# Kernel tuning notes

Hardware: AMD Instinct MI355X
Metric: run time of the kernel (lower is better)

The kernel has to match this reference:

```python
import jax, jax.numpy as jnp
import numpy as np

COSINE_SIM_SCALE = 8.0  # default scale in flash-cosine-sim-attention
LN_EPS = 1e-5
HEADS = 8

def _l2norm(t, eps=1e-12):
    return t * jax.lax.rsqrt(jnp.sum(t * t, axis=-1, keepdims=True) + eps)

def setup_inputs() -> dict:
    key = jax.random.key(0)
    k1, k2, k3 = jax.random.split(key, 3)
    b, n, dim = 2, 2048, 1024
    inner = 512  # heads * dim_head
    return {
        "x": jax.random.normal(k1, (b, n, dim), dtype=jnp.float32),
        "ln_w": jnp.ones((dim,), dtype=jnp.float32),
        "ln_b": jnp.zeros((dim,), dtype=jnp.float32),
        "w_qkv": jax.random.normal(k2, (dim, 3 * inner), dtype=jnp.float32) * 0.02,
        "w_out": jax.random.normal(k3, (inner, dim), dtype=jnp.float32) * 0.02,
    }

def reference(x, ln_w, ln_b, w_qkv, w_out):
    b, n, dim = x.shape
    h = HEADS
    # LayerNorm
    mu = jnp.mean(x, axis=-1, keepdims=True)
    var = jnp.mean(jnp.square(x - mu), axis=-1, keepdims=True)
    xn = (x - mu) * jax.lax.rsqrt(var + LN_EPS) * ln_w + ln_b
    # QKV projection, split into heads: b n (h d) -> b h n d
    qkv = xn @ w_qkv
    q, k, v = jnp.split(qkv, 3, axis=-1)
    def to_heads(t):
        return t.reshape(b, n, h, -1).transpose(0, 2, 1, 3)
    q, k, v = map(to_heads, (q, k, v))
    # cosine-sim attention: l2-normalize q, k then scaled dot product
    q = _l2norm(q)
    k = _l2norm(k)
    sim = jnp.einsum('bhid,bhjd->bhij', q, k) * COSINE_SIM_SCALE
    causal_mask = jnp.tril(jnp.ones((n, n), dtype=bool))
    sim = jnp.where(causal_mask, sim, jnp.finfo(sim.dtype).min)
    attn = jax.nn.softmax(sim, axis=-1)
    o = jnp.einsum('bhij,bhjd->bhid', attn, v)
    # b h n d -> b n (h d)
    o = o.transpose(0, 2, 1, 3).reshape(b, n, -1)
    return o @ w_out
```

## Files before the change

kernel.cpp:

```cpp
#include <hip/hip_runtime.h>
#include <hip/hip_bf16.h>

typedef __attribute__((ext_vector_type(8))) __bf16 bf16x8;
typedef __attribute__((ext_vector_type(4))) __bf16 bf16x4;
typedef __attribute__((ext_vector_type(4))) float f32x4;

#define B_     2
#define N_     2048
#define DIM_   1024
#define INNER_ 512
#define H_     8
#define DH_    64
#define ROWS_  (B_ * N_)
#define QKVN_  (3 * INNER_)
#define SEGROWS_ 5120
#define QSCALE_ 11.5415603f
#define MAXL2_  11.5415603f

static __device__ __forceinline__ f32x4 mfma16(bf16x8 a, bf16x8 b, f32x4 c) {
    return __builtin_amdgcn_mfma_f32_16x16x32_bf16(a, b, c, 0, 0, 0);
}

static __device__ __forceinline__ void gld_lds16(const void* g, void* l) {
    __builtin_amdgcn_global_load_lds((const __attribute__((address_space(1))) void*)g,
                                     (__attribute__((address_space(3))) void*)l, 16, 0, 0);
}

__global__ __launch_bounds__(256) void ln_kernel(const float* __restrict__ x,
                                                 const float* __restrict__ w,
                                                 const float* __restrict__ bb,
                                                 __bf16* __restrict__ xn) {
    int row = blockIdx.x;
    int tid = threadIdx.x;
    const float* xr = x + (size_t)row * DIM_;
    f32x4 xv = *reinterpret_cast<const f32x4*>(xr + tid * 4);
    float s  = xv.x + xv.y + xv.z + xv.w;
    float sq = xv.x * xv.x + xv.y * xv.y + xv.z * xv.z + xv.w * xv.w;
#pragma unroll
    for (int m = 1; m < 64; m <<= 1) {
        s  += __shfl_xor(s, m);
        sq += __shfl_xor(sq, m);
    }
    __shared__ float red[2][4];
    int wid = tid >> 6, lane = tid & 63;
    if (lane == 0) { red[0][wid] = s; red[1][wid] = sq; }
    __syncthreads();
    s  = red[0][0] + red[0][1] + red[0][2] + red[0][3];
    sq = red[1][0] + red[1][1] + red[1][2] + red[1][3];
    float mu   = s * (1.0f / DIM_);
    float var  = sq * (1.0f / DIM_) - mu * mu;
    float rstd = rsqrtf(var + 1e-5f);
    f32x4 wv = *reinterpret_cast<const f32x4*>(w  + tid * 4);
    f32x4 bv = *reinterpret_cast<const f32x4*>(bb + tid * 4);
    bf16x4 o;
#pragma unroll
    for (int j = 0; j < 4; ++j) o[j] = (__bf16)((xv[j] - mu) * rstd * wv[j] + bv[j]);
    *reinterpret_cast<bf16x4*>(xn + (size_t)row * DIM_ + tid * 4) = o;
}

__global__ __launch_bounds__(256) void transpose_both(const float* __restrict__ wqkv,
                                                      const float* __restrict__ wout,
                                                      __bf16* __restrict__ wqkvT,
                                                      __bf16* __restrict__ woutT) {
    __shared__ float t[64][65];
    int bid = blockIdx.x;
    const float* in; __bf16* out; int K, N, bx, by;
    if (bid < 384) { in = wqkv; out = wqkvT; K = DIM_;   N = QKVN_; bx = bid % 24; by = bid / 24; }
    else { bid -= 384; in = wout; out = woutT; K = INNER_; N = DIM_;  bx = bid % 16; by = bid / 16; }
    int n0 = bx * 64, k0 = by * 64;
    int w = threadIdx.x >> 6, lane = threadIdx.x & 63;
#pragma unroll
    for (int i = 0; i < 16; ++i) {
        int k = 16 * w + i;
        t[k][lane] = in[(size_t)(k0 + k) * N + n0 + lane];
    }
    __syncthreads();
#pragma unroll
    for (int i = 0; i < 16; ++i) {
        int n = 16 * w + i;
        out[(size_t)(n0 + n) * K + k0 + lane] = (__bf16)t[lane][n];
    }
}

__global__ __launch_bounds__(256) void gemm_qkv(const __bf16* __restrict__ A,
                                                const __bf16* __restrict__ Bt,
                                                __bf16* __restrict__ Qh,
                                                __bf16* __restrict__ Kh,
                                                __bf16* __restrict__ Vrow) {
    const int K = DIM_;
    __shared__ __bf16 As[2][128 * 32];
    __shared__ __bf16 Bs[2][128 * 32];
    int tid = threadIdx.x;
    int w = tid >> 6, lane = tid & 63;
    int lr = lane & 15, lg = lane >> 4;
    int m0 = blockIdx.y * 128, n0 = blockIdx.x * 128;
    int wm = (w >> 1) * 64, wn = (w & 1) * 64;
    int srow = tid >> 2, sc = tid & 3;
    const __bf16* Ab = A  + (size_t)m0 * K;
    const __bf16* Bb = Bt + (size_t)n0 * K;
    f32x4 acc[4][4];
#pragma unroll
    for (int mi = 0; mi < 4; ++mi)
#pragma unroll
        for (int ci = 0; ci < 4; ++ci) acc[mi][ci] = f32x4{0.f, 0.f, 0.f, 0.f};

    auto stage = [&](int buf, int k0) {
#pragma unroll
        for (int q = 0; q < 2; ++q) {
            int row = q * 64 + srow;
            int cs = sc ^ (row & 3);
            gld_lds16(Ab + (size_t)row * K + k0 + 8 * cs, &As[buf][(size_t)row * 32 + sc * 8]);
            gld_lds16(Bb + (size_t)row * K + k0 + 8 * cs, &Bs[buf][(size_t)row * 32 + sc * 8]);
        }
    };

    stage(0, 0);
    __syncthreads();
    int cur = 0;
    for (int k0 = 0; k0 < K; k0 += 32) {
        if (k0 + 32 < K) stage(cur ^ 1, k0 + 32);
        bf16x8 af[4], bfr[4];
#pragma unroll
        for (int mi = 0; mi < 4; ++mi) {
            int r = wm + 16 * mi + lr;
            af[mi] = *reinterpret_cast<const bf16x8*>(&As[cur][r * 32 + 8 * (lg ^ (r & 3))]);
        }
#pragma unroll
        for (int ci = 0; ci < 4; ++ci) {
            int r = wn + 16 * ci + lr;
            bfr[ci] = *reinterpret_cast<const bf16x8*>(&Bs[cur][r * 32 + 8 * (lg ^ (r & 3))]);
        }
#pragma unroll
        for (int mi = 0; mi < 4; ++mi)
#pragma unroll
            for (int ci = 0; ci < 4; ++ci)
                acc[mi][ci] = mfma16(af[mi], bfr[ci], acc[mi][ci]);
        __syncthreads();
        cur ^= 1;
    }
    int u = (n0 + wn) >> 6;
    bool isV = (u >= 16);
    float smul = (u < 8) ? QSCALE_ : 1.0f;
    __bf16* base;
    if (u < 8)       base = Qh   + (size_t)u * N_ * DH_;
    else if (u < 16) base = Kh   + (size_t)(u - 8) * N_ * DH_;
    else             base = Vrow + (size_t)(u - 16) * N_ * DH_;
#pragma unroll
    for (int mi = 0; mi < 4; ++mi)
#pragma unroll
        for (int r = 0; r < 4; ++r) {
            int grow = m0 + wm + 16 * mi + 4 * lg + r;
            int b = grow >> 11, n = grow & 2047;
            float sc2 = 1.0f;
            if (!isV) {
                float t = 0.f;
#pragma unroll
                for (int ci = 0; ci < 4; ++ci) t += acc[mi][ci][r] * acc[mi][ci][r];
#pragma unroll
                for (int m = 1; m < 16; m <<= 1) t += __shfl_xor(t, m);
                sc2 = rsqrtf(t + 1e-12f) * smul;
            }
            __bf16* dst = base + ((size_t)b * H_ * N_ + n) * DH_;
#pragma unroll
            for (int ci = 0; ci < 4; ++ci)
                dst[16 * ci + lr] = (__bf16)(acc[mi][ci][r] * sc2);
        }
}

__global__ __launch_bounds__(256) void gemm_out(const __bf16* __restrict__ A,
                                                const __bf16* __restrict__ Bt,
                                                float* __restrict__ C) {
    const int K = INNER_, N = DIM_;
    __shared__ __bf16 As[2][128 * 32];
    __shared__ __bf16 Bs[2][64 * 32];
    int tid = threadIdx.x;
    int w = tid >> 6, lane = tid & 63;
    int lr = lane & 15, lg = lane >> 4;
    int m0 = blockIdx.y * 128, n0 = blockIdx.x * 64;
    int wm = w * 32;
    int srow = tid >> 2, sc = tid & 3;
    const __bf16* Ab = A  + (size_t)m0 * K;
    const __bf16* Bb = Bt + (size_t)n0 * K;
    f32x4 acc[2][4];
#pragma unroll
    for (int mi = 0; mi < 2; ++mi)
#pragma unroll
        for (int ci = 0; ci < 4; ++ci) acc[mi][ci] = f32x4{0.f, 0.f, 0.f, 0.f};

    auto stage = [&](int buf, int k0) {
#pragma unroll
        for (int q = 0; q < 2; ++q) {
            int row = q * 64 + srow;
            int cs = sc ^ (row & 3);
            gld_lds16(Ab + (size_t)row * K + k0 + 8 * cs, &As[buf][(size_t)row * 32 + sc * 8]);
        }
        {
            int row = srow;
            int cs = sc ^ (row & 3);
            gld_lds16(Bb + (size_t)row * K + k0 + 8 * cs, &Bs[buf][(size_t)row * 32 + sc * 8]);
        }
    };

    stage(0, 0);
    __syncthreads();
    int cur = 0;
    for (int k0 = 0; k0 < K; k0 += 32) {
        if (k0 + 32 < K) stage(cur ^ 1, k0 + 32);
        bf16x8 af[2], bfr[4];
#pragma unroll
        for (int mi = 0; mi < 2; ++mi) {
            int r = wm + 16 * mi + lr;
            af[mi] = *reinterpret_cast<const bf16x8*>(&As[cur][r * 32 + 8 * (lg ^ (r & 3))]);
        }
#pragma unroll
        for (int ci = 0; ci < 4; ++ci) {
            int r = 16 * ci + lr;
            bfr[ci] = *reinterpret_cast<const bf16x8*>(&Bs[cur][r * 32 + 8 * (lg ^ (r & 3))]);
        }
#pragma unroll
        for (int mi = 0; mi < 2; ++mi)
#pragma unroll
            for (int ci = 0; ci < 4; ++ci)
                acc[mi][ci] = mfma16(af[mi], bfr[ci], acc[mi][ci]);
        __syncthreads();
        cur ^= 1;
    }
#pragma unroll
    for (int mi = 0; mi < 2; ++mi)
#pragma unroll
        for (int ci = 0; ci < 4; ++ci)
#pragma unroll
            for (int r = 0; r < 4; ++r)
                C[(size_t)(m0 + wm + 16 * mi + 4 * lg + r) * N + n0 + 16 * ci + lr] =
                    acc[mi][ci][r];
}

__global__ __launch_bounds__(256) void vtrans(const __bf16* __restrict__ Vrow,
                                              __bf16* __restrict__ Vt) {
    __shared__ __bf16 t[64][66];
    int bh = blockIdx.y, n0 = blockIdx.x * 64;
    int w = threadIdx.x >> 6, lane = threadIdx.x & 63;
#pragma unroll
    for (int i = 0; i < 16; ++i) {
        int nl = 16 * w + i;
        t[nl][lane] = Vrow[((size_t)bh * N_ + n0 + nl) * DH_ + lane];
    }
    __syncthreads();
#pragma unroll
    for (int i = 0; i < 16; ++i) {
        int d = 16 * w + i;
        Vt[(size_t)bh * DH_ * N_ + (size_t)d * N_ + n0 + lane] = t[lane][d];
    }
}

__global__ __launch_bounds__(256) void attn_kernel(const __bf16* __restrict__ Qh,
                                                   const __bf16* __restrict__ Kh,
                                                   const __bf16* __restrict__ Vt,
                                                   float* __restrict__ Opart,
                                                   float* __restrict__ lpart) {
    __shared__ __bf16 Ks[2][64 * 64];
    __shared__ __bf16 Vs[2][64 * 64];
    __shared__ __bf16 pl[4][16 * 64];
    int bh  = blockIdx.x & 15;
    int sid = blockIdx.x >> 4;
    int s, qt;
    if (sid < 32)      { s = 0; qt = 31 - sid; }
    else if (sid < 56) { s = 1; qt = 31 - (sid - 32); }
    else if (sid < 72) { s = 2; qt = 31 - (sid - 56); }
    else               { s = 3; qt = 31 - (sid - 72); }
    int jt0 = 8 * s;
    int jt1 = min(8 * s + 7, qt);
    int tid = threadIdx.x;
    int w = tid >> 6, lane = tid & 63;
    int lr = lane & 15, lg = lane >> 4;
    int qrow = qt * 64 + 16 * w;
    const __bf16* Qp = Qh + (size_t)bh * N_ * DH_;
    const __bf16* Kp = Kh + (size_t)bh * N_ * DH_;
    const __bf16* Vp = Vt + (size_t)bh * DH_ * N_;
    bf16x8 qf0 = *reinterpret_cast<const bf16x8*>(Qp + (size_t)(qrow + lr) * DH_ + 8 * lg);
    bf16x8 qf1 = *reinterpret_cast<const bf16x8*>(Qp + (size_t)(qrow + lr) * DH_ + 32 + 8 * lg);
    bf16x8 ones;
#pragma unroll
    for (int j = 0; j < 8; ++j) ones[j] = (__bf16)1.0f;
    f32x4 oacc[4];
    f32x4 oacc4 = f32x4{0.f, 0.f, 0.f, 0.f};
#pragma unroll
    for (int c = 0; c < 4; ++c) oacc[c] = f32x4{0.f, 0.f, 0.f, 0.f};
    int srow = tid >> 3, sc = tid & 7;

    auto stage = [&](int buf, int jb) {
#pragma unroll
        for (int q = 0; q < 2; ++q) {
            int row = q * 32 + srow;
            int cs = sc ^ (row & 7);
            gld_lds16(Kp + (size_t)(jb + row) * DH_ + 8 * cs,
                      &Ks[buf][(size_t)row * 64 + sc * 8]);
            gld_lds16(Vp + (size_t)row * N_ + jb + 8 * cs,
                      &Vs[buf][(size_t)row * 64 + sc * 8]);
        }
    };

    stage(0, jt0 * 64);
    __syncthreads();
    int cur = 0;
    for (int jt = jt0; jt <= jt1; ++jt) {
        int jb = jt * 64;
        if (jt < jt1) stage(cur ^ 1, jb + 64);
        const __bf16* ks = &Ks[cur][0];
        const __bf16* vs = &Vs[cur][0];
        f32x4 sm[4];
#pragma unroll
        for (int ch = 0; ch < 4; ++ch) {
            int row = 16 * ch + lr;
            bf16x8 k0 = *reinterpret_cast<const bf16x8*>(&ks[row * 64 + 8 * (lg ^ (row & 7))]);
            bf16x8 k1 = *reinterpret_cast<const bf16x8*>(&ks[row * 64 + 8 * ((4 + lg) ^ (row & 7))]);
            f32x4 t = f32x4{0.f, 0.f, 0.f, 0.f};
            t = mfma16(qf0, k0, t);
            t = mfma16(qf1, k1, t);
            sm[ch] = t;
        }
        f32x4 p[4];
        bool diag = (jt == qt);
#pragma unroll
        for (int ch = 0; ch < 4; ++ch)
#pragma unroll
            for (int r = 0; r < 4; ++r) {
                float pv = exp2f(sm[ch][r] - MAXL2_);
                if (diag) {
                    int qi = qrow + 4 * lg + r;
                    int j  = jb + 16 * ch + lr;
                    if (j > qi) pv = 0.f;
                }
                p[ch][r] = pv;
            }
        __bf16* plw = &pl[w][0];
#pragma unroll
        for (int ch = 0; ch < 4; ++ch)
#pragma unroll
            for (int r = 0; r < 4; ++r) {
                int row = 4 * lg + r, col = 16 * ch + lr;
                plw[row * 64 + (((col >> 3) ^ (row & 7)) << 3) + (col & 7)] = (__bf16)p[ch][r];
            }
        bf16x8 pf0 = *reinterpret_cast<const bf16x8*>(&plw[lr * 64 + ((lg ^ (lr & 7)) << 3)]);
        bf16x8 pf1 = *reinterpret_cast<const bf16x8*>(&plw[lr * 64 + (((4 + lg) ^ (lr & 7)) << 3)]);
#pragma unroll
        for (int dc = 0; dc < 4; ++dc) {
            int row = 16 * dc + lr;
            bf16x8 v0 = *reinterpret_cast<const bf16x8*>(&vs[row * 64 + 8 * (lg ^ (row & 7))]);
            bf16x8 v1 = *reinterpret_cast<const bf16x8*>(&vs[row * 64 + 8 * ((4 + lg) ^ (row & 7))]);
            oacc[dc] = mfma16(pf0, v0, oacc[dc]);
            oacc[dc] = mfma16(pf1, v1, oacc[dc]);
        }
        oacc4 = mfma16(pf0, ones, oacc4);
        oacc4 = mfma16(pf1, ones, oacc4);
        __syncthreads();
        cur ^= 1;
    }
    int soff = 2048 * s - 256 * s * (s - 1);
#pragma unroll
    for (int r = 0; r < 4; ++r) {
        int n = qrow + 4 * lg + r;
        size_t ridx = (size_t)bh * SEGROWS_ + soff + (n - 512 * s);
#pragma unroll
        for (int dc = 0; dc < 4; ++dc)
            Opart[ridx * 64 + 16 * dc + lr] = oacc[dc][r];
        if (lr == 0) lpart[ridx] = oacc4[r];
    }
}

__global__ __launch_bounds__(256) void combine_kernel(const float* __restrict__ Opart,
                                                      const float* __restrict__ lpart,
                                                      __bf16* __restrict__ Obp) {
    int gid = blockIdx.x * 4 + (threadIdx.x >> 6);
    int lane = threadIdx.x & 63;
    int bh = gid >> 11, n = gid & 2047;
    int smax = n >> 9;
    float acc = 0.f, lsum = 0.f;
#pragma unroll
    for (int s = 0; s < 4; ++s)
        if (s <= smax) {
            int soff = 2048 * s - 256 * s * (s - 1);
            size_t ridx = (size_t)bh * SEGROWS_ + soff + (n - 512 * s);
            acc  += Opart[ridx * 64 + lane];
            lsum += lpart[ridx];
        }
    int b = bh >> 3, h = bh & 7;
    Obp[((size_t)(b * N_ + n)) * INNER_ + h * DH_ + lane] = (__bf16)(acc / lsum);
}

extern "C" void kernel_launch(void* const* d_in, const int* in_sizes, int n_in,
                              void* d_out, int out_size, void* d_ws, size_t ws_size,
                              hipStream_t stream) {
    const float* x    = (const float*)d_in[0];
    const float* lnw  = (const float*)d_in[1];
    const float* lnb  = (const float*)d_in[2];
    const float* wqkv = (const float*)d_in[3];
    const float* wout = (const float*)d_in[4];
    float* out = (float*)d_out;

    char* ws = (char*)d_ws;
    size_t off = 0;
    auto alloc = [&](size_t bytes) -> char* {
        char* p = ws + off;
        off += (bytes + 255) & ~(size_t)255;
        return p;
    };
    __bf16* xn    = (__bf16*)alloc((size_t)ROWS_ * DIM_ * 2);
    __bf16* wqkvT = (__bf16*)alloc((size_t)QKVN_ * DIM_ * 2);
    __bf16* woutT = (__bf16*)alloc((size_t)DIM_ * INNER_ * 2);
    __bf16* Qhp   = (__bf16*)alloc((size_t)B_ * H_ * N_ * DH_ * 2);
    __bf16* Khp   = (__bf16*)alloc((size_t)B_ * H_ * N_ * DH_ * 2);
    __bf16* Vrow  = (__bf16*)alloc((size_t)B_ * H_ * N_ * DH_ * 2);
    __bf16* Vtp   = (__bf16*)alloc((size_t)B_ * H_ * DH_ * N_ * 2);
    __bf16* Obp   = (__bf16*)alloc((size_t)ROWS_ * INNER_ * 2);
    float*  Opart = (float*)alloc((size_t)B_ * H_ * SEGROWS_ * DH_ * 4);
    float*  lbuf  = (float*)alloc((size_t)B_ * H_ * SEGROWS_ * 4);
    if (off > ws_size) return;

    transpose_both<<<512, 256, 0, stream>>>(wqkv, wout, wqkvT, woutT);
    ln_kernel<<<ROWS_, 256, 0, stream>>>(x, lnw, lnb, xn);
    gemm_qkv<<<dim3(QKVN_ / 128, ROWS_ / 128), 256, 0, stream>>>(xn, wqkvT, Qhp, Khp, Vrow);
    vtrans<<<dim3(N_ / 64, B_ * H_), 256, 0, stream>>>(Vrow, Vtp);
    attn_kernel<<<1280, 256, 0, stream>>>(Qhp, Khp, Vtp, Opart, lbuf);
    combine_kernel<<<(ROWS_ * H_) / 4, 256, 0, stream>>>(Opart, lbuf, Obp);
    gemm_out<<<dim3(DIM_ / 64, ROWS_ / 128), 256, 0, stream>>>(Obp, woutT, out);
}
```

Baseline: 166.8 us.

## Retile QKV and output GEMMs to smaller tiles with K=64 steps and XCD-aware block mapping

The QKV GEMM moves from 128x128 tiles to 128x64 tiles, and the output GEMM from 128x64 to 64x64 tiles. Both now step K by 64 instead of 32, with an 8-way XOR swizzle in LDS. A 1D grid is remapped so that consecutive block IDs on each of the 8 XCDs cover neighbouring tiles, aiming for better L2 locality, more blocks to fill the CUs, and fewer barriers per K. The cost is less register-level reuse per wave, since each wave now computes fewer MFMA outputs per fragment load.

```diff
diff --git a/kernel.cpp b/kernel.cpp
--- a/kernel.cpp
+++ b/kernel.cpp
@@ -88,57 +88,72 @@
                                                 __bf16* __restrict__ Kh,
                                                 __bf16* __restrict__ Vrow) {
     const int K = DIM_;
-    __shared__ __bf16 As[2][128 * 32];
-    __shared__ __bf16 Bs[2][128 * 32];
+    __shared__ __bf16 As[2][128 * 64];
+    __shared__ __bf16 Bs[2][64 * 64];
+    int id = blockIdx.x;
+    int nid = (id & 7) * 96 + (id >> 3);
+    int bx = nid % 24, by = nid / 24;
     int tid = threadIdx.x;
     int w = tid >> 6, lane = tid & 63;
     int lr = lane & 15, lg = lane >> 4;
-    int m0 = blockIdx.y * 128, n0 = blockIdx.x * 128;
-    int wm = (w >> 1) * 64, wn = (w & 1) * 64;
-    int srow = tid >> 2, sc = tid & 3;
+    int m0 = by * 128, n0 = bx * 64;
+    int sr = tid >> 3;
+    int sc8 = tid & 7;
     const __bf16* Ab = A  + (size_t)m0 * K;
     const __bf16* Bb = Bt + (size_t)n0 * K;
-    f32x4 acc[4][4];
-#pragma unroll
-    for (int mi = 0; mi < 4; ++mi)
+    f32x4 acc[2][4];
+#pragma unroll
+    for (int mi = 0; mi < 2; ++mi)
 #pragma unroll
         for (int ci = 0; ci < 4; ++ci) acc[mi][ci] = f32x4{0.f, 0.f, 0.f, 0.f};
 
     auto stage = [&](int buf, int k0) {
 #pragma unroll
-        for (int q = 0; q < 2; ++q) {
-            int row = q * 64 + srow;
-            int cs = sc ^ (row & 3);
-            gld_lds16(Ab + (size_t)row * K + k0 + 8 * cs, &As[buf][(size_t)row * 32 + sc * 8]);
-            gld_lds16(Bb + (size_t)row * K + k0 + 8 * cs, &Bs[buf][(size_t)row * 32 + sc * 8]);
+        for (int i = 0; i < 4; ++i) {
+            int r = sr + i * 32;
+            int cs = sc8 ^ (r & 7);
+            gld_lds16(Ab + (size_t)r * K + k0 + 8 * cs, &As[buf][r * 64 + sc8 * 8]);
+        }
+#pragma unroll
+        for (int i = 0; i < 2; ++i) {
+            int r = sr + i * 32;
+            int cs = sc8 ^ (r & 7);
+            gld_lds16(Bb + (size_t)r * K + k0 + 8 * cs, &Bs[buf][r * 64 + sc8 * 8]);
         }
     };
 
     stage(0, 0);
     __syncthreads();
     int cur = 0;
-    for (int k0 = 0; k0 < K; k0 += 32) {
-        if (k0 + 32 < K) stage(cur ^ 1, k0 + 32);
-        bf16x8 af[4], bfr[4];
-#pragma unroll
-        for (int mi = 0; mi < 4; ++mi) {
-            int r = wm + 16 * mi + lr;
-            af[mi] = *reinterpret_cast<const bf16x8*>(&As[cur][r * 32 + 8 * (lg ^ (r & 3))]);
-        }
-#pragma unroll
-        for (int ci = 0; ci < 4; ++ci) {
-            int r = wn + 16 * ci + lr;
-            bfr[ci] = *reinterpret_cast<const bf16x8*>(&Bs[cur][r * 32 + 8 * (lg ^ (r & 3))]);
-        }
-#pragma unroll
-        for (int mi = 0; mi < 4; ++mi)
-#pragma unroll
-            for (int ci = 0; ci < 4; ++ci)
-                acc[mi][ci] = mfma16(af[mi], bfr[ci], acc[mi][ci]);
+    for (int k0 = 0; k0 < K; k0 += 64) {
+        if (k0 + 64 < K) stage(cur ^ 1, k0 + 64);
+        bf16x8 af[2][2], bfr[2][4];
+#pragma unroll
+        for (int kk = 0; kk < 2; ++kk) {
+#pragma unroll
+            for (int mi = 0; mi < 2; ++mi) {
+                int r = w * 32 + 16 * mi + lr;
+                af[kk][mi] = *reinterpret_cast<const bf16x8*>(
+                    &As[cur][r * 64 + 8 * ((kk * 4 + lg) ^ (r & 7))]);
+            }
+#pragma unroll
+            for (int ci = 0; ci < 4; ++ci) {
+                int r = 16 * ci + lr;
+                bfr[kk][ci] = *reinterpret_cast<const bf16x8*>(
+                    &Bs[cur][r * 64 + 8 * ((kk * 4 + lg) ^ (r & 7))]);
+            }
+        }
+#pragma unroll
+        for (int kk = 0; kk < 2; ++kk)
+#pragma unroll
+            for (int mi = 0; mi < 2; ++mi)
+#pragma unroll
+                for (int ci = 0; ci < 4; ++ci)
+                    acc[mi][ci] = mfma16(af[kk][mi], bfr[kk][ci], acc[mi][ci]);
         __syncthreads();
         cur ^= 1;
     }
-    int u = (n0 + wn) >> 6;
+    int u = bx;
     bool isV = (u >= 16);
     float smul = (u < 8) ? QSCALE_ : 1.0f;
     __bf16* base;
@@ -146,10 +161,10 @@
     else if (u < 16) base = Kh   + (size_t)(u - 8) * N_ * DH_;
     else             base = Vrow + (size_t)(u - 16) * N_ * DH_;
 #pragma unroll
-    for (int mi = 0; mi < 4; ++mi)
+    for (int mi = 0; mi < 2; ++mi)
 #pragma unroll
         for (int r = 0; r < 4; ++r) {
-            int grow = m0 + wm + 16 * mi + 4 * lg + r;
+            int grow = m0 + w * 32 + 16 * mi + 4 * lg + r;
             int b = grow >> 11, n = grow & 2047;
             float sc2 = 1.0f;
             if (!isV) {
@@ -171,68 +186,63 @@
                                                 const __bf16* __restrict__ Bt,
                                                 float* __restrict__ C) {
     const int K = INNER_, N = DIM_;
-    __shared__ __bf16 As[2][128 * 32];
-    __shared__ __bf16 Bs[2][64 * 32];
+    __shared__ __bf16 As[2][64 * 64];
+    __shared__ __bf16 Bs[2][64 * 64];
+    int id = blockIdx.x;
+    int nid = (id & 7) * 128 + (id >> 3);
+    int bx = nid % 16, by = nid / 16;
     int tid = threadIdx.x;
     int w = tid >> 6, lane = tid & 63;
     int lr = lane & 15, lg = lane >> 4;
-    int m0 = blockIdx.y * 128, n0 = blockIdx.x * 64;
-    int wm = w * 32;
-    int srow = tid >> 2, sc = tid & 3;
+    int m0 = by * 64, n0 = bx * 64;
+    int sr = tid >> 3, sc8 = tid & 7;
     const __bf16* Ab = A  + (size_t)m0 * K;
     const __bf16* Bb = Bt + (size_t)n0 * K;
-    f32x4 acc[2][4];
-#pragma unroll
-    for (int mi = 0; mi < 2; ++mi)
-#pragma unroll
-        for (int ci = 0; ci < 4; ++ci) acc[mi][ci] = f32x4{0.f, 0.f, 0.f, 0.f};
+    f32x4 acc[4];
+#pragma unroll
+    for (int ci = 0; ci < 4; ++ci) acc[ci] = f32x4{0.f, 0.f, 0.f, 0.f};
 
     auto stage = [&](int buf, int k0) {
 #pragma unroll
-        for (int q = 0; q < 2; ++q) {
-            int row = q * 64 + srow;
-            int cs = sc ^ (row & 3);
-            gld_lds16(Ab + (size_t)row * K + k0 + 8 * cs, &As[buf][(size_t)row * 32 + sc * 8]);
-        }
-        {
-            int row = srow;
-            int cs = sc ^ (row & 3);
-            gld_lds16(Bb + (size_t)row * K + k0 + 8 * cs, &Bs[buf][(size_t)row * 32 + sc * 8]);
+        for (int i = 0; i < 2; ++i) {
+            int r = sr + i * 32;
+            int cs = sc8 ^ (r & 7);
+            gld_lds16(Ab + (size_t)r * K + k0 + 8 * cs, &As[buf][r * 64 + sc8 * 8]);
+            gld_lds16(Bb + (size_t)r * K + k0 + 8 * cs, &Bs[buf][r * 64 + sc8 * 8]);
         }
     };
 
     stage(0, 0);
     __syncthreads();
     int cur = 0;
-    for (int k0 = 0; k0 < K; k0 += 32) {
-        if (k0 + 32 < K) stage(cur ^ 1, k0 + 32);
-        bf16x8 af[2], bfr[4];
-#pragma unroll
-        for (int mi = 0; mi < 2; ++mi) {
-            int r = wm + 16 * mi + lr;
-            af[mi] = *reinterpret_cast<const bf16x8*>(&As[cur][r * 32 + 8 * (lg ^ (r & 3))]);
-        }
-#pragma unroll
-        for (int ci = 0; ci < 4; ++ci) {
-            int r = 16 * ci + lr;
-            bfr[ci] = *reinterpret_cast<const bf16x8*>(&Bs[cur][r * 32 + 8 * (lg ^ (r & 3))]);
-        }
-#pragma unroll
-        for (int mi = 0; mi < 2; ++mi)
+    for (int k0 = 0; k0 < K; k0 += 64) {
+        if (k0 + 64 < K) stage(cur ^ 1, k0 + 64);
+        bf16x8 af[2], bfr[2][4];
+#pragma unroll
+        for (int kk = 0; kk < 2; ++kk) {
+            int r = w * 16 + lr;
+            af[kk] = *reinterpret_cast<const bf16x8*>(
+                &As[cur][r * 64 + 8 * ((kk * 4 + lg) ^ (r & 7))]);
+#pragma unroll
+            for (int ci = 0; ci < 4; ++ci) {
+                int rb = 16 * ci + lr;
+                bfr[kk][ci] = *reinterpret_cast<const bf16x8*>(
+                    &Bs[cur][rb * 64 + 8 * ((kk * 4 + lg) ^ (rb & 7))]);
+            }
+        }
+#pragma unroll
+        for (int kk = 0; kk < 2; ++kk)
 #pragma unroll
             for (int ci = 0; ci < 4; ++ci)
-                acc[mi][ci] = mfma16(af[mi], bfr[ci], acc[mi][ci]);
+                acc[ci] = mfma16(af[kk], bfr[kk][ci], acc[ci]);
         __syncthreads();
         cur ^= 1;
     }
 #pragma unroll
-    for (int mi = 0; mi < 2; ++mi)
-#pragma unroll
-        for (int ci = 0; ci < 4; ++ci)
-#pragma unroll
-            for (int r = 0; r < 4; ++r)
-                C[(size_t)(m0 + wm + 16 * mi + 4 * lg + r) * N + n0 + 16 * ci + lr] =
-                    acc[mi][ci][r];
+    for (int ci = 0; ci < 4; ++ci)
+#pragma unroll
+        for (int r = 0; r < 4; ++r)
+            C[(size_t)(m0 + w * 16 + 4 * lg + r) * N + n0 + 16 * ci + lr] = acc[ci][r];
 }
 
 __global__ __launch_bounds__(256) void vtrans(const __bf16* __restrict__ Vrow,
@@ -419,9 +429,9 @@
 
     transpose_both<<<512, 256, 0, stream>>>(wqkv, wout, wqkvT, woutT);
     ln_kernel<<<ROWS_, 256, 0, stream>>>(x, lnw, lnb, xn);
-    gemm_qkv<<<dim3(QKVN_ / 128, ROWS_ / 128), 256, 0, stream>>>(xn, wqkvT, Qhp, Khp, Vrow);
+    gemm_qkv<<<768, 256, 0, stream>>>(xn, wqkvT, Qhp, Khp, Vrow);
     vtrans<<<dim3(N_ / 64, B_ * H_), 256, 0, stream>>>(Vrow, Vtp);
     attn_kernel<<<1280, 256, 0, stream>>>(Qhp, Khp, Vtp, Opart, lbuf);
     combine_kernel<<<(ROWS_ * H_) / 4, 256, 0, stream>>>(Opart, lbuf, Obp);
-    gemm_out<<<dim3(DIM_ / 64, ROWS_ / 128), 256, 0, stream>>>(Obp, woutT, out);
-}
+    gemm_out<<<1024, 256, 0, stream>>>(Obp, woutT, out);
+}
```

Result: faster. 153.2 us (-8.2%).
